# Performance work log

Measured on AMD Instinct MI355X. Metric: run time of the kernel, lower is better.

The kernel has to match this reference:

```python
import jax, jax.numpy as jnp
import numpy as np

D = 256        # d_model
NH = 8         # nhead
L = 2          # num_layers
FF = 1024      # dim_feedforward
HD = D // NH   # head dim
LN_EPS = 1e-5
M_EPS = 1e-9


def setup_inputs() -> dict:
    key = jax.random.key(0)
    ks = jax.random.split(key, 8)
    B, N, E = 8, 1024, 16384
    s = 0.02
    inp = {
        "H": jax.random.normal(ks[0], (B, N, D), jnp.float32),
        "edge_index": jax.random.randint(ks[1], (B, 2, E), 0, N),
        "m": jax.random.uniform(ks[2], (B, E), jnp.float32),
        # transformer encoder params, stacked over layers
        "Wqkv": jax.random.normal(ks[3], (L, 3 * D, D), jnp.float32) * s,
        "bqkv": jnp.zeros((L, 3 * D), jnp.float32),
        "Wo": jax.random.normal(ks[4], (L, D, D), jnp.float32) * s,
        "bo": jnp.zeros((L, D), jnp.float32),
        "ln1_w": jnp.ones((L, D), jnp.float32),
        "ln1_b": jnp.zeros((L, D), jnp.float32),
        "W1": jax.random.normal(ks[5], (L, FF, D), jnp.float32) * s,
        "b1": jnp.zeros((L, FF), jnp.float32),
        "W2": jax.random.normal(ks[6], (L, D, FF), jnp.float32) * s,
        "b2": jnp.zeros((L, D), jnp.float32),
        "ln2_w": jnp.ones((L, D), jnp.float32),
        "ln2_b": jnp.zeros((L, D), jnp.float32),
        "lnf_w": jnp.ones((D,), jnp.float32),
        "lnf_b": jnp.zeros((D,), jnp.float32),
    }
    return inp


def layer_norm(x, w, b):
    mu = jnp.mean(x, axis=-1, keepdims=True)
    var = jnp.mean(jnp.square(x - mu), axis=-1, keepdims=True)
    return (x - mu) * jax.lax.rsqrt(var + LN_EPS) * w + b


def build_bias(edge_index, m, N):
    # per-graph: -inf everywhere, 0 on diag, log(m+eps) symmetrically on edges
    bias = jnp.full((N, N), -jnp.inf, jnp.float32)
    d = jnp.arange(N)
    bias = bias.at[d, d].set(0.0)
    bv = jnp.log(m + M_EPS)
    row, col = edge_index[0], edge_index[1]
    bias = bias.at[row, col].set(bv)
    bias = bias.at[col, row].set(bv)
    return bias


def mha(x, bias, Wqkv, bqkv, Wo, bo):
    B, N, d = x.shape
    qkv = x @ Wqkv.T + bqkv                          # [B,N,3D]
    q, k, v = jnp.split(qkv, 3, axis=-1)
    def heads(t):
        return t.reshape(B, N, NH, HD).transpose(0, 2, 1, 3)  # [B,NH,N,HD]
    q, k, v = heads(q), heads(k), heads(v)
    scores = jnp.einsum("bhnd,bhmd->bhnm", q, k) / np.sqrt(HD)
    scores = scores + bias[:, None]                  # same bias for all heads
    attn = jax.nn.softmax(scores, axis=-1)
    out = jnp.einsum("bhnm,bhmd->bhnd", attn, v)
    out = out.transpose(0, 2, 1, 3).reshape(B, N, d)
    return out @ Wo.T + bo


def reference(H, edge_index, m, Wqkv, bqkv, Wo, bo, ln1_w, ln1_b, W1, b1,
              W2, b2, ln2_w, ln2_b, lnf_w, lnf_b):
    B, N, _ = H.shape
    bias = jax.vmap(lambda ei, mm: build_bias(ei, mm, N))(edge_index, m)  # [B,N,N]
    x = H
    for l in range(L):  # small fixed layer count
        a = mha(x, bias, Wqkv[l], bqkv[l], Wo[l], bo[l])
        x = layer_norm(x + a, ln1_w[l], ln1_b[l])
        f = jax.nn.gelu(x @ W1[l].T + b1[l], approximate=False) @ W2[l].T + b2[l]
        x = layer_norm(x + f, ln2_w[l], ln2_b[l])
    return layer_norm(x, lnf_w, lnf_b)
```

## Files before the change

### kernel.cpp

```cpp
#include <hip/hip_runtime.h>
#include <hip/hip_bf16.h>
#include <math.h>

typedef __bf16 bf16_t;
typedef __attribute__((ext_vector_type(8))) __bf16 bf16x8;
typedef __attribute__((ext_vector_type(4))) __bf16 bf16x4;
typedef __attribute__((ext_vector_type(4))) float f32x4;

#define BATCH 8
#define NTOK 1024
#define NEDGE 16384
#define CAP 96

__device__ __forceinline__ void gload_lds16(const void* g, void* l) {
  __builtin_amdgcn_global_load_lds(
      (const __attribute__((address_space(1))) unsigned int*)(uintptr_t)g,
      (__attribute__((address_space(3))) unsigned int*)(unsigned int)(uintptr_t)l,
      16, 0, 0);
}

__global__ void k_pre(int4* __restrict__ cnt,
                      const float* __restrict__ H, const float* __restrict__ Wqkv,
                      const float* __restrict__ Wo, const float* __restrict__ W1,
                      const float* __restrict__ W2, bf16_t* __restrict__ xb,
                      bf16_t* __restrict__ wqkvb, bf16_t* __restrict__ wob,
                      bf16_t* __restrict__ w1b, bf16_t* __restrict__ w2b) {
  int i = blockIdx.x * 256 + threadIdx.x;
  if (blockIdx.x < 8) {
    int4 z = {0, 0, 0, 0};
    cnt[i] = z;
  }
  const float* s; bf16_t* d; int off;
  if (i < 524288)      { s = H;    d = xb;    off = i; }
  else if (i < 622592) { s = Wqkv; d = wqkvb; off = i - 524288; }
  else if (i < 655360) { s = Wo;   d = wob;   off = i - 622592; }
  else if (i < 786432) { s = W1;   d = w1b;   off = i - 655360; }
  else if (i < 917504) { s = W2;   d = w2b;   off = i - 786432; }
  else return;
  float4 v = ((const float4*)s)[off];
  bf16x4 o;
  o[0] = (bf16_t)v.x; o[1] = (bf16_t)v.y; o[2] = (bf16_t)v.z; o[3] = (bf16_t)v.w;
  ((bf16x4*)d)[off] = o;
}

__global__ void k_scatter2(const int* __restrict__ ei, int* __restrict__ cnt,
                           int* __restrict__ ent) {
  int idx = blockIdx.x * 256 + threadIdx.x;
  if (idx >= BATCH * NEDGE) return;
  int b = idx >> 14;
  int e = idx & (NEDGE - 1);
  const int* eb = ei + (size_t)b * 2 * NEDGE;
  int r = eb[e], c = eb[NEDGE + e];
  int rowr = (b << 10) + r, rowc = (b << 10) + c;
  int q = atomicAdd(cnt + rowr, 1);
  if (q < CAP) ent[rowr * CAP + q] = ((e + 1) << 10) | c;
  q = atomicAdd(cnt + rowc, 1);
  if (q < CAP) ent[rowc * CAP + q] = ((NEDGE + e + 1) << 10) | r;
}

__global__ __launch_bounds__(256) void k_build2(
    const int* __restrict__ cnt, const int* __restrict__ ent,
    const float* __restrict__ mptr,
    int* __restrict__ nbcol, float* __restrict__ nbval, int* __restrict__ nbcnt) {
  const int w = threadIdx.x >> 6;
  const int l = threadIdx.x & 63;
  const int row = blockIdx.x * 4 + w;
  const int i = row & 1023;
  const int b = row >> 10;
  __shared__ int sE[4][CAP];
  __shared__ int sW[4][CAP];
  const int n = min(cnt[row], CAP);
  for (int j = l; j < n; j += 64) sE[w][j] = ent[(size_t)row * CAP + j];
  __syncthreads();

  bool dcov_l = false;
  bool win[2] = {false, false};
  int myc[2], myp[2];
#pragma unroll
  for (int s = 0; s < 2; ++s) {
    int k = s * 64 + l;
    if (k < n) {
      int pk = sE[w][k], ck = pk & 1023;
      myc[s] = ck; myp[s] = pk;
      bool wn = true;
      for (int j = 0; j < n; ++j) {
        int pj = sE[w][j];
        if ((pj & 1023) == ck && pj > pk) wn = false;
      }
      win[s] = wn;
      sW[w][k] = wn ? 1 : 0;
      if (ck == i) dcov_l = true;
    }
  }
  const bool dcov = __any(dcov_l);
  unsigned long long m0 = __ballot(win[0]);
  unsigned long long m1 = __ballot(win[1]);
  if (l == 0) nbcnt[row] = __popcll(m0) + __popcll(m1) + (dcov ? 0 : 1);

#pragma unroll
  for (int s = 0; s < 2; ++s) {
    int k = s * 64 + l;
    if (k < n && win[s]) {
      int pos = 0;
      for (int j = 0; j < n; ++j)
        if (sW[w][j] && (sE[w][j] & 1023) < myc[s]) ++pos;
      if (!dcov && i < myc[s]) ++pos;
      int e = ((myp[s] >> 10) - 1) & (NEDGE - 1);
      float v = logf(mptr[(size_t)b * NEDGE + e] + 1e-9f);
      if (pos < CAP) {
        nbcol[(size_t)row * CAP + pos] = myc[s];
        nbval[(size_t)row * CAP + pos] = v;
      }
    }
  }
  if (!dcov && l == 0) {
    int pos = 0;
    for (int j = 0; j < n; ++j)
      if (sW[w][j] && (sE[w][j] & 1023) < i) ++pos;
    nbcol[(size_t)row * CAP + pos] = i;
    nbval[(size_t)row * CAP + pos] = 0.f;
  }
}

template <int EPI, int BM>
__global__ __launch_bounds__(256) void gemm_bt(
    const bf16_t* __restrict__ A, const bf16_t* __restrict__ Bw,
    const float* __restrict__ bias, bf16_t* __restrict__ Cb,
    int M, int N, int K) {
  constexpr int MI = BM / 32;
  __shared__ bf16_t As[2][BM * 64];
  __shared__ bf16_t Bs[2][128 * 64];
  const int t = threadIdx.x;
  const int l = t & 63;
  const int w = t >> 6;
  const int wr = w >> 1, wc = w & 1;
  const int per = gridDim.x >> 3;
  const int g2 = (blockIdx.x & 7) * per + (blockIdx.x >> 3);
  const int NX = N >> 7;
  const int bm = (g2 / NX) * BM, bn = (g2 % NX) * 128;

  f32x4 acc[MI][4] = {};

  auto stage = [&](int buf, int k0) {
#pragma unroll
    for (int i = 0; i < BM / 32; ++i) {
      int idx = i * 2048 + t * 8;
      int row = idx >> 6, col = idx & 63;
      gload_lds16(A + (size_t)(bm + row) * K + (k0 + col), (void*)(&As[buf][0] + i * 2048 + w * 512));
    }
#pragma unroll
    for (int i = 0; i < 4; ++i) {
      int idx = i * 2048 + t * 8;
      int row = idx >> 6, col = idx & 63;
      gload_lds16(Bw + (size_t)(bn + row) * K + (k0 + col), (void*)(&Bs[buf][0] + i * 2048 + w * 512));
    }
  };

  const int nt = K >> 6;
  stage(0, 0);
  asm volatile("s_waitcnt vmcnt(0)" ::: "memory");
  __syncthreads();
  for (int kt = 0; kt < nt; ++kt) {
    const int cur = kt & 1;
    if (kt + 1 < nt) stage(cur ^ 1, (kt + 1) << 6);
#pragma unroll
    for (int kk = 0; kk < 2; ++kk) {
      bf16x8 af[MI], bfr[4];
#pragma unroll
      for (int mi = 0; mi < MI; ++mi)
        af[mi] = *(const bf16x8*)(&As[cur][0] + (wr * (BM / 2) + mi * 16 + (l & 15)) * 64 + kk * 32 + (l >> 4) * 8);
#pragma unroll
      for (int ni = 0; ni < 4; ++ni)
        bfr[ni] = *(const bf16x8*)(&Bs[cur][0] + (wc * 64 + ni * 16 + (l & 15)) * 64 + kk * 32 + (l >> 4) * 8);
#pragma unroll
      for (int mi = 0; mi < MI; ++mi)
#pragma unroll
        for (int ni = 0; ni < 4; ++ni)
          acc[mi][ni] = __builtin_amdgcn_mfma_f32_16x16x32_bf16(af[mi], bfr[ni], acc[mi][ni], 0, 0, 0);
    }
    asm volatile("s_waitcnt vmcnt(0)" ::: "memory");
    __syncthreads();
  }

  const int r0 = (l >> 4) * 4;
  const int cc = l & 15;
#pragma unroll
  for (int mi = 0; mi < MI; ++mi) {
#pragma unroll
    for (int ni = 0; ni < 4; ++ni) {
      int col = bn + wc * 64 + ni * 16 + cc;
      float bv = bias[col];
#pragma unroll
      for (int r = 0; r < 4; ++r) {
        int row = bm + wr * (BM / 2) + mi * 16 + r0 + r;
        float v = acc[mi][ni][r] + bv;
        if (EPI == 1)
          v = 0.5f * v * (1.f + erff(v * 0.70710678118654752f));
        Cb[(size_t)row * N + col] = (bf16_t)v;
      }
    }
  }
}

__global__ __launch_bounds__(256) void k_attn_oproj(
    const bf16_t* __restrict__ qkvb,
    const int* __restrict__ nbcol, const float* __restrict__ nbval,
    const int* __restrict__ nbcnt,
    const bf16_t* __restrict__ Wo, const float* __restrict__ bo,
    const bf16_t* __restrict__ residb,
    const float* __restrict__ lnw, const float* __restrict__ lnb,
    bf16_t* __restrict__ xbout) {
  __shared__ __align__(16) char smem[36096];
  bf16_t* Bs    = (bf16_t*)smem;
  bf16_t* ao    = (bf16_t*)(smem + 16384);
  float*  s_s   = (float*)(smem + 20608);
  int*    s_col = (int*)(smem + 33024);
  float*  s_bia = (float*)(smem + 34560);
  float*  E     = (float*)(smem + 16384);
  const int t = threadIdx.x, l = t & 63, w = t >> 6;
  const int b = blockIdx.x & 7;
  const int bm = (b << 10) + (blockIdx.x >> 3) * 8;

  auto stageB = [&](int k0) {
#pragma unroll
    for (int i = 0; i < 4; ++i) {
      int rr = (w * 4 + i) * 16 + (l >> 2), ch = (l & 3) * 8;
      gload_lds16(Wo + (size_t)rr * 256 + (k0 + ch), (void*)(Bs + (w * 4 + i) * 512));
    }
  };
  stageB(0);

  const float scale = 0.17677669529663687f;
  const int h1 = l & 7;
  for (int rr = 0; rr < 2; ++rr) {
    const int row = bm + w * 2 + rr;
    const int deg = nbcnt[row];
    asm volatile("s_waitcnt lgkmcnt(0)" ::: "memory");
    for (int j = l; j < deg; j += 64) {
      s_col[w * 96 + j] = nbcol[(size_t)row * CAP + j];
      s_bia[w * 96 + j] = nbval[(size_t)row * CAP + j];
    }
    float q[32];
    {
      const bf16x8* qp = (const bf16x8*)(qkvb + (size_t)row * 768 + h1 * 32);
#pragma unroll
      for (int u = 0; u < 4; ++u) {
        bf16x8 t8 = qp[u];
#pragma unroll
        for (int j = 0; j < 8; ++j) q[u * 8 + j] = (float)t8[j];
      }
    }
    asm volatile("s_waitcnt lgkmcnt(0)" ::: "memory");

    const int nit = (deg + 7) >> 3;
    float mx = -INFINITY;
    for (int it = 0; it < nit; ++it) {
      int idx = it * 8 + (l >> 3);
      float sc = -INFINITY;
      if (idx < deg) {
        int col = s_col[w * 96 + idx];
        const bf16x8* kr = (const bf16x8*)(qkvb + ((size_t)((b << 10) + col)) * 768 + 256 + h1 * 32);
        float d = 0.f;
#pragma unroll
        for (int u = 0; u < 4; ++u) {
          bf16x8 kv = kr[u];
#pragma unroll
          for (int j = 0; j < 8; ++j) d += (float)kv[j] * q[u * 8 + j];
        }
        sc = d * scale + s_bia[w * 96 + idx];
        s_s[(w * 8 + h1) * 97 + idx] = sc;
      }
      mx = fmaxf(mx, sc);
    }
#pragma unroll
    for (int o = 8; o < 64; o <<= 1) mx = fmaxf(mx, __shfl_xor(mx, o));
    asm volatile("s_waitcnt lgkmcnt(0)" ::: "memory");
    float lsum = 0.f;
    for (int it = 0; it < nit; ++it) {
      int idx = it * 8 + (l >> 3);
      if (idx < deg) {
        float p = __expf(s_s[(w * 8 + h1) * 97 + idx] - mx);
        s_s[(w * 8 + h1) * 97 + idx] = p;
        lsum += p;
      }
    }
#pragma unroll
    for (int o = 8; o < 64; o <<= 1) lsum += __shfl_xor(lsum, o);
    const int h3 = l >> 3;
    float den = __shfl(lsum, h3);
    asm volatile("s_waitcnt lgkmcnt(0)" ::: "memory");
    float a0 = 0.f, a1 = 0.f, a2 = 0.f, a3 = 0.f;
    const bf16_t* vbase = qkvb + ((size_t)(b << 10)) * 768 + 512 + l * 4;
#pragma unroll 4
    for (int idx = 0; idx < deg; ++idx) {
      float p = s_s[(w * 8 + h3) * 97 + idx];
      bf16x4 vv = *(const bf16x4*)(vbase + (size_t)s_col[w * 96 + idx] * 768);
      a0 += p * (float)vv[0]; a1 += p * (float)vv[1];
      a2 += p * (float)vv[2]; a3 += p * (float)vv[3];
    }
    float rden = 1.f / den;
    bf16x4 o4;
    o4[0] = (bf16_t)(a0 * rden); o4[1] = (bf16_t)(a1 * rden);
    o4[2] = (bf16_t)(a2 * rden); o4[3] = (bf16_t)(a3 * rden);
    *(bf16x4*)(ao + (w * 2 + rr) * 264 + l * 4) = o4;
  }
  asm volatile("s_waitcnt vmcnt(0) lgkmcnt(0)" ::: "memory");
  __syncthreads();

  f32x4 acc[4] = {};
  for (int kt = 0; kt < 8; ++kt) {
    bf16x8 af = *(const bf16x8*)(ao + (l & 15) * 264 + kt * 32 + (l >> 4) * 8);
    __builtin_amdgcn_s_setprio(1);
#pragma unroll
    for (int ni = 0; ni < 4; ++ni) {
      bf16x8 bfr = *(const bf16x8*)(Bs + (w * 64 + ni * 16 + (l & 15)) * 32 + (l >> 4) * 8);
      acc[ni] = __builtin_amdgcn_mfma_f32_16x16x32_bf16(af, bfr, acc[ni], 0, 0, 0);
    }
    __builtin_amdgcn_s_setprio(0);
    __syncthreads();
    if (kt < 7) {
      stageB((kt + 1) * 32);
      asm volatile("s_waitcnt vmcnt(0)" ::: "memory");
      __syncthreads();
    }
  }

  const int r0 = (l >> 4) * 4;
  const int cc = l & 15;
#pragma unroll
  for (int ni = 0; ni < 4; ++ni) {
    int col = w * 64 + ni * 16 + cc;
    float bv = bo[col];
#pragma unroll
    for (int r = 0; r < 4; ++r)
      E[(r0 + r) * 258 + col] = acc[ni][r] + bv;
  }
  __syncthreads();

  const int row = t >> 5;
  const int sub = t & 31;
  const float* ep = E + row * 258 + sub * 8;
  const bf16_t* rp = residb + (size_t)(bm + row) * 256 + sub * 8;
  float v[8];
  float s = 0.f;
#pragma unroll
  for (int j = 0; j < 2; ++j) {
    float4 a4 = ((const float4*)ep)[j];
    bf16x4 r4 = ((const bf16x4*)rp)[j];
    v[j * 4 + 0] = a4.x + (float)r4[0]; v[j * 4 + 1] = a4.y + (float)r4[1];
    v[j * 4 + 2] = a4.z + (float)r4[2]; v[j * 4 + 3] = a4.w + (float)r4[3];
    s += v[j * 4 + 0] + v[j * 4 + 1] + v[j * 4 + 2] + v[j * 4 + 3];
  }
#pragma unroll
  for (int o = 1; o < 32; o <<= 1) s += __shfl_xor(s, o);
  float mu = s * (1.f / 256.f);
  float e2 = 0.f;
#pragma unroll
  for (int j = 0; j < 8; ++j) { float d = v[j] - mu; e2 += d * d; }
#pragma unroll
  for (int o = 1; o < 32; o <<= 1) e2 += __shfl_xor(e2, o);
  float rs = rsqrtf(e2 * (1.f / 256.f) + 1e-5f);
  bf16_t* xbo = xbout + (size_t)(bm + row) * 256 + sub * 8;
#pragma unroll
  for (int j = 0; j < 2; ++j) {
    float4 w4 = ((const float4*)(lnw + sub * 8))[j];
    float4 b4 = ((const float4*)(lnb + sub * 8))[j];
    bf16x4 ob;
    ob[0] = (bf16_t)((v[j * 4 + 0] - mu) * rs * w4.x + b4.x);
    ob[1] = (bf16_t)((v[j * 4 + 1] - mu) * rs * w4.y + b4.y);
    ob[2] = (bf16_t)((v[j * 4 + 2] - mu) * rs * w4.z + b4.z);
    ob[3] = (bf16_t)((v[j * 4 + 3] - mu) * rs * w4.w + b4.w);
    ((bf16x4*)xbo)[j] = ob;
  }
}

template <int FIN>
__global__ __launch_bounds__(256) void gemm_ln(
    const bf16_t* __restrict__ A, const bf16_t* __restrict__ Bw,
    const float* __restrict__ bias, const bf16_t* __restrict__ residb,
    const float* __restrict__ lnw, const float* __restrict__ lnb,
    const float* __restrict__ lnfw, const float* __restrict__ lnfb,
    bf16_t* __restrict__ xbout, float* __restrict__ outf, int K) {
  __shared__ __align__(16) char smem[69632];
  bf16_t* As = (bf16_t*)smem;
  bf16_t* Bs = (bf16_t*)(smem + 4096);
  float*  E  = (float*)smem;
  const int t = threadIdx.x;
  const int l = t & 63;
  const int w = t >> 6;
  const int per = gridDim.x >> 3;
  const int g2 = (blockIdx.x & 7) * per + (blockIdx.x >> 3);
  const int bm = g2 * 16;

  f32x4 acc[4] = {};

  auto stage = [&](int buf, int k0) {
    if (w < 2) {
      int row = w * 8 + (l >> 3), col = (l & 7) * 8;
      gload_lds16(A + (size_t)(bm + row) * K + (k0 + col), (void*)(As + buf * 1024 + w * 512));
    }
#pragma unroll
    for (int i = 0; i < 8; ++i) {
      int rr = (w * 8 + i) * 8 + (l >> 3), col = (l & 7) * 8;
      gload_lds16(Bw + (size_t)rr * K + (k0 + col), (void*)(Bs + buf * 16384 + (w * 8 + i) * 512));
    }
  };

  const int nt = K >> 6;
  stage(0, 0);
  asm volatile("s_waitcnt vmcnt(0)" ::: "memory");
  __syncthreads();
  for (int kt = 0; kt < nt; ++kt) {
    const int cur = kt & 1;
    if (kt + 1 < nt) stage(cur ^ 1, (kt + 1) << 6);
#pragma unroll
    for (int kk = 0; kk < 2; ++kk) {
      bf16x8 af = *(const bf16x8*)(As + cur * 1024 + (l & 15) * 64 + kk * 32 + (l >> 4) * 8);
#pragma unroll
      for (int ni = 0; ni < 4; ++ni) {
        bf16x8 bfr = *(const bf16x8*)(Bs + cur * 16384 + (w * 64 + ni * 16 + (l & 15)) * 64 + kk * 32 + (l >> 4) * 8);
        acc[ni] = __builtin_amdgcn_mfma_f32_16x16x32_bf16(af, bfr, acc[ni], 0, 0, 0);
      }
    }
    asm volatile("s_waitcnt vmcnt(0)" ::: "memory");
    __syncthreads();
  }

  const int r0 = (l >> 4) * 4;
  const int cc = l & 15;
#pragma unroll
  for (int ni = 0; ni < 4; ++ni) {
    int col = w * 64 + ni * 16 + cc;
    float bv = bias[col];
#pragma unroll
    for (int r = 0; r < 4; ++r)
      E[(r0 + r) * 258 + col] = acc[ni][r] + bv;
  }
  __syncthreads();

  const int row = t >> 4;
  const int sub = t & 15;
  const float* ep = E + row * 258 + sub * 16;
  const bf16_t* rp = residb + (size_t)(bm + row) * 256 + sub * 16;
  float v[16];
  float s = 0.f;
#pragma unroll
  for (int j = 0; j < 4; ++j) {
    float4 a4 = ((const float4*)ep)[j];
    bf16x4 r4 = ((const bf16x4*)rp)[j];
    v[j * 4 + 0] = a4.x + (float)r4[0]; v[j * 4 + 1] = a4.y + (float)r4[1];
    v[j * 4 + 2] = a4.z + (float)r4[2]; v[j * 4 + 3] = a4.w + (float)r4[3];
    s += v[j * 4 + 0] + v[j * 4 + 1] + v[j * 4 + 2] + v[j * 4 + 3];
  }
#pragma unroll
  for (int o = 1; o < 16; o <<= 1) s += __shfl_xor(s, o);
  float mu = s * (1.f / 256.f);
  float e2 = 0.f;
#pragma unroll
  for (int j = 0; j < 16; ++j) { float d = v[j] - mu; e2 += d * d; }
#pragma unroll
  for (int o = 1; o < 16; o <<= 1) e2 += __shfl_xor(e2, o);
  float rs = rsqrtf(e2 * (1.f / 256.f) + 1e-5f);
  float y[16];
#pragma unroll
  for (int j = 0; j < 4; ++j) {
    float4 w4 = ((const float4*)(lnw + sub * 16))[j];
    float4 b4 = ((const float4*)(lnb + sub * 16))[j];
    y[j * 4 + 0] = (v[j * 4 + 0] - mu) * rs * w4.x + b4.x;
    y[j * 4 + 1] = (v[j * 4 + 1] - mu) * rs * w4.y + b4.y;
    y[j * 4 + 2] = (v[j * 4 + 2] - mu) * rs * w4.z + b4.z;
    y[j * 4 + 3] = (v[j * 4 + 3] - mu) * rs * w4.w + b4.w;
  }
  if (FIN == 0) {
    bf16_t* xbo = xbout + (size_t)(bm + row) * 256 + sub * 16;
#pragma unroll
    for (int j = 0; j < 4; ++j) {
      bf16x4 ob;
      ob[0] = (bf16_t)y[j * 4 + 0]; ob[1] = (bf16_t)y[j * 4 + 1];
      ob[2] = (bf16_t)y[j * 4 + 2]; ob[3] = (bf16_t)y[j * 4 + 3];
      ((bf16x4*)xbo)[j] = ob;
    }
  } else {
    float s2 = 0.f;
#pragma unroll
    for (int j = 0; j < 16; ++j) s2 += y[j];
#pragma unroll
    for (int o = 1; o < 16; o <<= 1) s2 += __shfl_xor(s2, o);
    float mu2 = s2 * (1.f / 256.f);
    float q2 = 0.f;
#pragma unroll
    for (int j = 0; j < 16; ++j) { float d = y[j] - mu2; q2 += d * d; }
#pragma unroll
    for (int o = 1; o < 16; o <<= 1) q2 += __shfl_xor(q2, o);
    float rs2 = rsqrtf(q2 * (1.f / 256.f) + 1e-5f);
    float* xo = outf + (size_t)(bm + row) * 256 + sub * 16;
#pragma unroll
    for (int j = 0; j < 4; ++j) {
      float4 w4 = ((const float4*)(lnfw + sub * 16))[j];
      float4 b4 = ((const float4*)(lnfb + sub * 16))[j];
      float4 o4 = {(y[j * 4 + 0] - mu2) * rs2 * w4.x + b4.x,
                   (y[j * 4 + 1] - mu2) * rs2 * w4.y + b4.y,
                   (y[j * 4 + 2] - mu2) * rs2 * w4.z + b4.z,
                   (y[j * 4 + 3] - mu2) * rs2 * w4.w + b4.w};
      ((float4*)xo)[j] = o4;
    }
  }
}

extern "C" void kernel_launch(void* const* d_in, const int* in_sizes, int n_in,
                              void* d_out, int out_size, void* d_ws, size_t ws_size,
                              hipStream_t stream) {
  const float* H    = (const float*)d_in[0];
  const int*   ei   = (const int*)d_in[1];
  const float* m    = (const float*)d_in[2];
  const float* Wqkv = (const float*)d_in[3];
  const float* bqkv = (const float*)d_in[4];
  const float* Wo   = (const float*)d_in[5];
  const float* bo   = (const float*)d_in[6];
  const float* ln1w = (const float*)d_in[7];
  const float* ln1b = (const float*)d_in[8];
  const float* W1   = (const float*)d_in[9];
  const float* b1   = (const float*)d_in[10];
  const float* W2   = (const float*)d_in[11];
  const float* b2   = (const float*)d_in[12];
  const float* ln2w = (const float*)d_in[13];
  const float* ln2b = (const float*)d_in[14];
  const float* lnfw = (const float*)d_in[15];
  const float* lnfb = (const float*)d_in[16];

  char* ws = (char*)d_ws;
  size_t off = 0;
  auto alloc = [&](size_t bytes) {
    void* p = ws + off;
    off += (bytes + 255) & ~(size_t)255;
    return p;
  };

  int*    cnt   = (int*)alloc((size_t)BATCH * NTOK * 4);
  int*    ent   = (int*)alloc((size_t)BATCH * NTOK * CAP * 4);
  int*    nbcol = (int*)alloc((size_t)BATCH * NTOK * CAP * 4);
  float*  nbval = (float*)alloc((size_t)BATCH * NTOK * CAP * 4);
  int*    nbcnt = (int*)alloc((size_t)BATCH * NTOK * 4);
  bf16_t* qkvb  = (bf16_t*)alloc((size_t)8192 * 768 * 2);
  bf16_t* wqkvb = (bf16_t*)alloc((size_t)2 * 768 * 256 * 2);
  bf16_t* wob   = (bf16_t*)alloc((size_t)2 * 256 * 256 * 2);
  bf16_t* w1b   = (bf16_t*)alloc((size_t)2 * 1024 * 256 * 2);
  bf16_t* w2b   = (bf16_t*)alloc((size_t)2 * 256 * 1024 * 2);
  bf16_t* xb    = (bf16_t*)alloc((size_t)8192 * 256 * 2);
  bf16_t* x1b   = (bf16_t*)alloc((size_t)8192 * 256 * 2);
  bf16_t* ffb   = (bf16_t*)alloc((size_t)8192 * 1024 * 2);

  k_pre<<<3584, 256, 0, stream>>>((int4*)cnt, H, Wqkv, Wo, W1, W2,
                                  xb, wqkvb, wob, w1b, w2b);
  k_scatter2<<<(BATCH * NEDGE + 255) / 256, 256, 0, stream>>>(ei, cnt, ent);
  k_build2<<<BATCH * NTOK / 4, 256, 0, stream>>>(cnt, ent, m, nbcol, nbval, nbcnt);

  for (int lyr = 0; lyr < 2; ++lyr) {
    gemm_bt<3, 64><<<(768 / 128) * (8192 / 64), 256, 0, stream>>>(
        xb, wqkvb + (size_t)lyr * 768 * 256, bqkv + lyr * 768, qkvb, 8192, 768, 256);
    k_attn_oproj<<<1024, 256, 0, stream>>>(
        qkvb, nbcol, nbval, nbcnt,
        wob + (size_t)lyr * 256 * 256, bo + lyr * 256, xb,
        ln1w + lyr * 256, ln1b + lyr * 256, x1b);
    gemm_bt<1, 128><<<(1024 / 128) * (8192 / 128), 256, 0, stream>>>(
        x1b, w1b + (size_t)lyr * 1024 * 256, b1 + lyr * 1024, ffb, 8192, 1024, 256);
    if (lyr == 0) {
      gemm_ln<0><<<512, 256, 0, stream>>>(
          ffb, w2b + (size_t)lyr * 256 * 1024, b2 + lyr * 256, x1b,
          ln2w + lyr * 256, ln2b + lyr * 256, nullptr, nullptr, xb, nullptr, 1024);
    } else {
      gemm_ln<1><<<512, 256, 0, stream>>>(
          ffb, w2b + (size_t)lyr * 256 * 1024, b2 + lyr * 256, x1b,
          ln2w + lyr * 256, ln2b + lyr * 256, lnfw, lnfb, nullptr, (float*)d_out, 1024);
    }
  }
}
```

Before: 178.6 us.

## Retile FF2+LayerNorm GEMM to 8-row tiles with 128 threads, shrink FF1 tiles

The fused FF2 GEMM + LayerNorm kernel now handles 8 rows per block with 2 waves instead of 16 rows with 4 waves. It uses a 32-wide K step, a hardcoded K, half the LDS and 1024 blocks instead of 512. This should give more parallelism and occupancy across CUs. The cost is that the 16x16 MFMA tiles are now half-empty on the A side, so half the matrix work is discarded, and more blocks each reload the full weight tiles. It also adds s_setprio around the MFMA loop and shrinks the FF1 GEMM row tile from 128 to 64.

```diff
diff --git a/kernel.cpp b/kernel.cpp
--- a/kernel.cpp
+++ b/kernel.cpp
@@ -375,66 +375,67 @@
 }
 
 template <int FIN>
-__global__ __launch_bounds__(256) void gemm_ln(
+__global__ __launch_bounds__(128) void gemm_ln(
     const bf16_t* __restrict__ A, const bf16_t* __restrict__ Bw,
     const float* __restrict__ bias, const bf16_t* __restrict__ residb,
     const float* __restrict__ lnw, const float* __restrict__ lnb,
     const float* __restrict__ lnfw, const float* __restrict__ lnfb,
-    bf16_t* __restrict__ xbout, float* __restrict__ outf, int K) {
-  __shared__ __align__(16) char smem[69632];
+    bf16_t* __restrict__ xbout, float* __restrict__ outf) {
+  constexpr int K = 1024;
+  __shared__ __align__(16) char smem[34816];
   bf16_t* As = (bf16_t*)smem;
-  bf16_t* Bs = (bf16_t*)(smem + 4096);
+  bf16_t* Bs = (bf16_t*)(smem + 2048);
   float*  E  = (float*)smem;
   const int t = threadIdx.x;
   const int l = t & 63;
   const int w = t >> 6;
   const int per = gridDim.x >> 3;
   const int g2 = (blockIdx.x & 7) * per + (blockIdx.x >> 3);
-  const int bm = g2 * 16;
-
-  f32x4 acc[4] = {};
+  const int bm = g2 * 8;
+
+  f32x4 acc[8] = {};
 
   auto stage = [&](int buf, int k0) {
-    if (w < 2) {
-      int row = w * 8 + (l >> 3), col = (l & 7) * 8;
-      gload_lds16(A + (size_t)(bm + row) * K + (k0 + col), (void*)(As + buf * 1024 + w * 512));
+    if (w == 0 && l < 32) {
+      gload_lds16(A + (size_t)(bm + (l >> 2)) * K + (k0 + (l & 3) * 8), (void*)(As + buf * 256));
     }
 #pragma unroll
     for (int i = 0; i < 8; ++i) {
-      int rr = (w * 8 + i) * 8 + (l >> 3), col = (l & 7) * 8;
-      gload_lds16(Bw + (size_t)rr * K + (k0 + col), (void*)(Bs + buf * 16384 + (w * 8 + i) * 512));
+      int rr = (w * 8 + i) * 16 + (l >> 2), ch = (l & 3) * 8;
+      gload_lds16(Bw + (size_t)rr * K + (k0 + ch), (void*)(Bs + buf * 8192 + (w * 8 + i) * 512));
     }
   };
 
-  const int nt = K >> 6;
   stage(0, 0);
   asm volatile("s_waitcnt vmcnt(0)" ::: "memory");
   __syncthreads();
-  for (int kt = 0; kt < nt; ++kt) {
+#pragma unroll 4
+  for (int kt = 0; kt < 32; ++kt) {
     const int cur = kt & 1;
-    if (kt + 1 < nt) stage(cur ^ 1, (kt + 1) << 6);
-#pragma unroll
-    for (int kk = 0; kk < 2; ++kk) {
-      bf16x8 af = *(const bf16x8*)(As + cur * 1024 + (l & 15) * 64 + kk * 32 + (l >> 4) * 8);
-#pragma unroll
-      for (int ni = 0; ni < 4; ++ni) {
-        bf16x8 bfr = *(const bf16x8*)(Bs + cur * 16384 + (w * 64 + ni * 16 + (l & 15)) * 64 + kk * 32 + (l >> 4) * 8);
-        acc[ni] = __builtin_amdgcn_mfma_f32_16x16x32_bf16(af, bfr, acc[ni], 0, 0, 0);
-      }
-    }
+    if (kt + 1 < 32) stage(cur ^ 1, (kt + 1) * 32);
+    bf16x8 af = *(const bf16x8*)(As + cur * 256 + (l & 15) * 32 + (l >> 4) * 8);
+    __builtin_amdgcn_s_setprio(1);
+#pragma unroll
+    for (int ni = 0; ni < 8; ++ni) {
+      bf16x8 bfr = *(const bf16x8*)(Bs + cur * 8192 + (w * 128 + ni * 16 + (l & 15)) * 32 + (l >> 4) * 8);
+      acc[ni] = __builtin_amdgcn_mfma_f32_16x16x32_bf16(af, bfr, acc[ni], 0, 0, 0);
+    }
+    __builtin_amdgcn_s_setprio(0);
     asm volatile("s_waitcnt vmcnt(0)" ::: "memory");
     __syncthreads();
   }
 
   const int r0 = (l >> 4) * 4;
   const int cc = l & 15;
-#pragma unroll
-  for (int ni = 0; ni < 4; ++ni) {
-    int col = w * 64 + ni * 16 + cc;
-    float bv = bias[col];
-#pragma unroll
-    for (int r = 0; r < 4; ++r)
-      E[(r0 + r) * 258 + col] = acc[ni][r] + bv;
+  if (r0 < 8) {
+#pragma unroll
+    for (int ni = 0; ni < 8; ++ni) {
+      int col = w * 128 + ni * 16 + cc;
+      float bv = bias[col];
+#pragma unroll
+      for (int r = 0; r < 4; ++r)
+        E[(r0 + r) * 258 + col] = acc[ni][r] + bv;
+    }
   }
   __syncthreads();
 
@@ -562,16 +563,16 @@
         qkvb, nbcol, nbval, nbcnt,
         wob + (size_t)lyr * 256 * 256, bo + lyr * 256, xb,
         ln1w + lyr * 256, ln1b + lyr * 256, x1b);
-    gemm_bt<1, 128><<<(1024 / 128) * (8192 / 128), 256, 0, stream>>>(
+    gemm_bt<1, 64><<<(1024 / 128) * (8192 / 64), 256, 0, stream>>>(
         x1b, w1b + (size_t)lyr * 1024 * 256, b1 + lyr * 1024, ffb, 8192, 1024, 256);
     if (lyr == 0) {
-      gemm_ln<0><<<512, 256, 0, stream>>>(
+      gemm_ln<0><<<1024, 128, 0, stream>>>(
           ffb, w2b + (size_t)lyr * 256 * 1024, b2 + lyr * 256, x1b,
-          ln2w + lyr * 256, ln2b + lyr * 256, nullptr, nullptr, xb, nullptr, 1024);
+          ln2w + lyr * 256, ln2b + lyr * 256, nullptr, nullptr, xb, nullptr);
     } else {
-      gemm_ln<1><<<512, 256, 0, stream>>>(
+      gemm_ln<1><<<1024, 128, 0, stream>>>(
           ffb, w2b + (size_t)lyr * 256 * 1024, b2 + lyr * 256, x1b,
-          ln2w + lyr * 256, ln2b + lyr * 256, lnfw, lnfb, nullptr, (float*)d_out, 1024);
-    }
-  }
-}
+          ln2w + lyr * 256, ln2b + lyr * 256, lnfw, lnfb, nullptr, (float*)d_out);
+    }
+  }
+}
```

New measurement: 214.8 us. +20.2%, slower.
